# Kernel tuning notes

Hardware: AMD Instinct MI355X
Metric: run time of the kernel (lower is better)

The kernel has to match this reference:

```python
import jax, jax.numpy as jnp
import numpy as np

EMBED_DIM = 1024
NUM_HEADS = 16
HEAD_DIM = EMBED_DIM // NUM_HEADS


def setup_inputs() -> dict:
    key = jax.random.key(0)
    ks = jax.random.split(key, 7)
    B, S, D = 8, 1024, EMBED_DIM
    scale = 1.0 / np.sqrt(D)
    x = jax.random.normal(ks[0], (B, S, D), dtype=jnp.float32)
    Wq = jax.random.normal(ks[1], (D, D), dtype=jnp.float32) * scale
    Wk = jax.random.normal(ks[2], (D, D), dtype=jnp.float32) * scale
    Wv = jax.random.normal(ks[3], (D, D), dtype=jnp.float32) * scale
    bq = jax.random.normal(ks[4], (D,), dtype=jnp.float32) * 0.01
    bk = jax.random.normal(ks[5], (D,), dtype=jnp.float32) * 0.01
    bv = jax.random.normal(ks[6], (D,), dtype=jnp.float32) * 0.01
    return {"x": x, "Wq": Wq, "Wk": Wk, "Wv": Wv, "bq": bq, "bk": bk, "bv": bv}


def reference(x, Wq, Wk, Wv, bq, bk, bv):
    B, S, D = x.shape
    H, Hd = NUM_HEADS, HEAD_DIM
    # torch nn.Linear: y = x @ W.T + b
    q = (x @ Wq.T + bq).reshape(B, S, H, Hd).transpose(0, 2, 1, 3)  # [B,H,S,Hd]
    k = (x @ Wk.T + bk).reshape(B, S, H, Hd).transpose(0, 2, 1, 3)
    v = (x @ Wv.T + bv).reshape(B, S, H, Hd).transpose(0, 2, 1, 3)
    scale = Hd ** -0.5
    scores = jnp.einsum('bhqd,bhkd->bhqk', q, k) * scale  # [B,H,S,S]
    attn = jax.nn.softmax(scores, axis=-1)
    # dropout_rate = 0.0 -> identity; out_proj is never applied in the source forward
    ctx = jnp.einsum('bhqk,bhkd->bhqd', attn, v)  # [B,H,S,Hd]
    return ctx.transpose(0, 2, 1, 3).reshape(B, S, D)
```

## Files before the change

kernel.cpp:

```cpp
#include <hip/hip_runtime.h>
#include <hip/hip_bf16.h>
#include <cstdint>
#include <cstddef>


typedef __attribute__((ext_vector_type(8))) short bf16x8;
typedef __attribute__((ext_vector_type(8))) unsigned short u16x8;
typedef __attribute__((ext_vector_type(4))) float f32x4;
typedef __attribute__((ext_vector_type(16))) float f32x16;
typedef __attribute__((ext_vector_type(4))) unsigned int u32x4;
typedef __attribute__((ext_vector_type(2))) unsigned int u32x2;

typedef const __attribute__((address_space(1))) void* gptr_t;
typedef __attribute__((address_space(3))) void* lptr_t;

#define LOG2E 1.44269504088896340736f

__device__ __forceinline__ unsigned short f2bf(float f) {
  unsigned int u = __float_as_uint(f);
  u += 0x7fffu + ((u >> 16) & 1u);
  return (unsigned short)(u >> 16);
}

__device__ __forceinline__ unsigned int pack_bf16x2(float lo, float hi) {
  const __hip_bfloat162 h = __float22bfloat162_rn(float2{lo, hi});
  unsigned int u;
  __builtin_memcpy(&u, &h, 4);
  return u;
}

__device__ __forceinline__ float vmax16(const f32x16& v) {
  float a = fmaxf(fmaxf(v[0], v[1]), v[2]);
  float b = fmaxf(fmaxf(v[3], v[4]), v[5]);
  float c = fmaxf(fmaxf(v[6], v[7]), v[8]);
  float d = fmaxf(fmaxf(v[9], v[10]), v[11]);
  float e = fmaxf(fmaxf(v[12], v[13]), v[14]);
  float f = fmaxf(fmaxf(a, b), v[15]);
  float h = fmaxf(fmaxf(c, d), e);
  return fmaxf(f, h);
}

__global__ void cvt_all(const float* __restrict__ x, const float* __restrict__ wq,
                        const float* __restrict__ wk, const float* __restrict__ wv,
                        unsigned short* __restrict__ Xb, unsigned short* __restrict__ Wb) {
  const int b = blockIdx.x;
  const float* src;
  unsigned short* dst;
  int i;
  if (b < 8192) {
    src = x; dst = Xb; i = b * 256 + threadIdx.x;
  } else {
    const int s = b - 8192;
    const int sel = s >> 10;
    src = (sel == 0) ? wq : (sel == 1) ? wk : wv;
    dst = Wb + (size_t)sel * 1048576;
    i = (s & 1023) * 256 + threadIdx.x;
  }
  float4 v = reinterpret_cast<const float4*>(src)[i];
  ushort4 o;
  o.x = f2bf(v.x); o.y = f2bf(v.y); o.z = f2bf(v.z); o.w = f2bf(v.w);
  reinterpret_cast<ushort4*>(dst)[i] = o;
}

__global__ __launch_bounds__(256) void qkv_gemm(
    const unsigned short* __restrict__ Xb, const unsigned short* __restrict__ Wb,
    const float* __restrict__ bq, const float* __restrict__ bk,
    const float* __restrict__ bv,
    unsigned short* __restrict__ Qo, unsigned short* __restrict__ Ko,
    unsigned short* __restrict__ Vo) {
  __shared__ unsigned short As[128 * 32];
  __shared__ unsigned short Bs[128 * 32];

  const int tid = threadIdx.x;
  const int lane = tid & 63;
  const int w = tid >> 6;
  const int wr = w >> 1, wc = w & 1;
  const int bm = blockIdx.x & 63;
  const int bn = blockIdx.x >> 6;

  const f32x4 vzero = {0.f, 0.f, 0.f, 0.f};
  f32x4 acc[4][4];
#pragma unroll
  for (int m = 0; m < 4; ++m)
#pragma unroll
    for (int n = 0; n < 4; ++n) acc[m][n] = vzero;

  const int c0 = w * 2, c1 = w * 2 + 1;
  const int srow0 = c0 * 16 + (lane >> 2);
  const int srow1 = c1 * 16 + (lane >> 2);
  const int scol = (lane & 3) * 8;
  const unsigned short* gA0 = Xb + (size_t)(bm * 128 + srow0) * 1024 + scol;
  const unsigned short* gA1 = Xb + (size_t)(bm * 128 + srow1) * 1024 + scol;
  const unsigned short* gB0 = Wb + (size_t)(bn * 128 + srow0) * 1024 + scol;
  const unsigned short* gB1 = Wb + (size_t)(bn * 128 + srow1) * 1024 + scol;
  char* lA0 = (char*)As + c0 * 1024;
  char* lA1 = (char*)As + c1 * 1024;
  char* lB0 = (char*)Bs + c0 * 1024;
  char* lB1 = (char*)Bs + c1 * 1024;

  const int aoff = (wr * 64 + (lane & 15)) * 64 + (lane >> 4) * 16;
  const int boff = (wc * 64 + (lane & 15)) * 64 + (lane >> 4) * 16;

  for (int kt = 0; kt < 32; ++kt) {
    const int k0 = kt * 32;
    __builtin_amdgcn_global_load_lds((gptr_t)(gA0 + k0), (lptr_t)lA0, 16, 0, 0);
    __builtin_amdgcn_global_load_lds((gptr_t)(gA1 + k0), (lptr_t)lA1, 16, 0, 0);
    __builtin_amdgcn_global_load_lds((gptr_t)(gB0 + k0), (lptr_t)lB0, 16, 0, 0);
    __builtin_amdgcn_global_load_lds((gptr_t)(gB1 + k0), (lptr_t)lB1, 16, 0, 0);
    __syncthreads();

    bf16x8 a[4], b[4];
#pragma unroll
    for (int m = 0; m < 4; ++m)
      a[m] = *reinterpret_cast<const bf16x8*>((const char*)As + aoff + m * 16 * 64);
#pragma unroll
    for (int n = 0; n < 4; ++n)
      b[n] = *reinterpret_cast<const bf16x8*>((const char*)Bs + boff + n * 16 * 64);
#pragma unroll
    for (int m = 0; m < 4; ++m)
#pragma unroll
      for (int n = 0; n < 4; ++n)
        acc[m][n] = __builtin_amdgcn_mfma_f32_16x16x32_bf16(a[m], b[n], acc[m][n], 0, 0, 0);
    __syncthreads();
  }

  const int t = bn >> 3;
  const float* bias = (t == 0) ? bq : (t == 1) ? bk : bv;
  unsigned short* dst = (t == 0) ? Qo : (t == 1) ? Ko : Vo;
  const float sc = (t == 0) ? 0.125f : 1.0f;
#pragma unroll
  for (int n = 0; n < 4; ++n) {
    const int gn = bn * 128 + wc * 64 + n * 16 + (lane & 15);
    const int d = gn & 1023;
    const int h = d >> 6, hd = d & 63;
    const float bias_v = bias[d];
#pragma unroll
    for (int m = 0; m < 4; ++m) {
      const int gm0 = bm * 128 + wr * 64 + m * 16 + ((lane >> 4) << 2);
      const int bb = gm0 >> 10;
      const int s0 = gm0 & 1023;
#pragma unroll
      for (int r = 0; r < 4; ++r) {
        dst[(((size_t)bb * 16 + h) * 1024 + (size_t)(s0 + r)) * 64 + hd] =
            f2bf((acc[m][n][r] + bias_v) * sc);
      }
    }
  }
}

__global__ __launch_bounds__(256) void transpose_v(
    const unsigned short* __restrict__ Vn, unsigned short* __restrict__ Vt) {
  __shared__ __align__(16) unsigned short T[64][72];
  const int tid = threadIdx.x;
  const int head = blockIdx.x & 127;
  const int st = blockIdx.x >> 7;
  const unsigned short* src = Vn + (size_t)head * 65536 + (size_t)st * 64 * 64;
  unsigned short* dst = Vt + (size_t)head * 65536 + (size_t)st * 64;
#pragma unroll
  for (int i = 0; i < 2; ++i) {
    const int idx = tid + i * 256;
    const int r = idx >> 3, ch = idx & 7;
    u16x8 v = *reinterpret_cast<const u16x8*>(src + r * 64 + ch * 8);
#pragma unroll
    for (int j = 0; j < 8; ++j)
      T[ch * 8 + j][r ^ (ch << 3)] = (unsigned short)v[j];
  }
  __syncthreads();
#pragma unroll
  for (int i = 0; i < 2; ++i) {
    const int idx = tid + i * 256;
    const int d = idx >> 3, ch = idx & 7;
    u16x8 v = *reinterpret_cast<const u16x8*>(&T[d][(ch ^ (d >> 3)) << 3]);
    *reinterpret_cast<u16x8*>(dst + (size_t)d * 1024 + ch * 8) = v;
  }
}

__global__ __launch_bounds__(512, 4) void attn32(
    const unsigned short* __restrict__ Q, const unsigned short* __restrict__ K,
    const unsigned short* __restrict__ Vt, float* __restrict__ out) {
  __shared__ __align__(16) char smem[3][16384];

  const int tid = threadIdx.x;
  const int lane = tid & 63;
  const int ln31 = lane & 31;
  const int g = lane >> 5;
  const int w = tid >> 6;
  const int head = blockIdx.x & 127;
  const int qt = blockIdx.x >> 7;

  const unsigned short* Qh = Q + (size_t)head * 65536;
  const unsigned short* Kh = K + (size_t)head * 65536;
  const unsigned short* Vh = Vt + (size_t)head * 65536;

  const int qrow = qt * 256 + w * 32 + ln31;
  bf16x8 qf[4];
#pragma unroll
  for (int dc = 0; dc < 4; ++dc)
    qf[dc] = *reinterpret_cast<const bf16x8*>(Qh + (size_t)qrow * 64 + dc * 16 + g * 8);
  asm volatile("s_waitcnt vmcnt(0)" ::: "memory");

  const int lb = w * 1024 + lane * 16;
  const int r = lb >> 7;
  const int c = ((((lb >> 4) & 7) ^ (r & 7)) << 3);
  const unsigned short* gK = Kh + r * 64 + c;
  const unsigned short* gV = Vh + r * 1024 + c;

#pragma unroll
  for (int pt = 0; pt < 2; ++pt) {
    char* b0 = smem[pt] + w * 1024;
    __builtin_amdgcn_global_load_lds((gptr_t)(gK + pt * 4096), (lptr_t)b0, 16, 0, 0);
    __builtin_amdgcn_global_load_lds((gptr_t)(gV + pt * 64), (lptr_t)(b0 + 8192), 16, 0, 0);
  }

  float m_ = -3e38f, l_ = 0.f;
  f32x16 acc0, acc1, z16;
#pragma unroll
  for (int i = 0; i < 16; ++i) { acc0[i] = 0.f; acc1[i] = 0.f; z16[i] = 0.f; }

  const int swz = (ln31 & 7) << 4;
  const int rowb0 = ln31 * 128;
  int boff[4];
#pragma unroll
  for (int dc = 0; dc < 4; ++dc) boff[dc] = ((((dc << 1) | g) << 4) ^ swz);

  for (int kt = 0; kt < 16; ++kt) {
    if (kt < 15) {
      asm volatile("s_waitcnt vmcnt(2)" ::: "memory");
    } else {
      asm volatile("s_waitcnt vmcnt(0)" ::: "memory");
    }
    __builtin_amdgcn_s_barrier();
    __builtin_amdgcn_sched_barrier(0);

    if (kt < 14) {
      char* nb = smem[(kt + 2) % 3] + w * 1024;
      __builtin_amdgcn_global_load_lds((gptr_t)(gK + (kt + 2) * 4096), (lptr_t)nb, 16, 0, 0);
      __builtin_amdgcn_global_load_lds((gptr_t)(gV + (kt + 2) * 64), (lptr_t)(nb + 8192), 16, 0, 0);
    }

    const char* Kb_ = smem[kt % 3] + rowb0;
    const char* Vb_ = Kb_ + 8192;

    f32x16 s0, s1;
    __builtin_amdgcn_s_setprio(1);
    {
      bf16x8 kf0 = *reinterpret_cast<const bf16x8*>(Kb_ + boff[0]);
      bf16x8 kf1 = *reinterpret_cast<const bf16x8*>(Kb_ + 4096 + boff[0]);
      s0 = __builtin_amdgcn_mfma_f32_32x32x16_bf16(kf0, qf[0], z16, 0, 0, 0);
      s1 = __builtin_amdgcn_mfma_f32_32x32x16_bf16(kf1, qf[0], z16, 0, 0, 0);
    }
#pragma unroll
    for (int dc = 1; dc < 4; ++dc) {
      bf16x8 kf0 = *reinterpret_cast<const bf16x8*>(Kb_ + boff[dc]);
      bf16x8 kf1 = *reinterpret_cast<const bf16x8*>(Kb_ + 4096 + boff[dc]);
      s0 = __builtin_amdgcn_mfma_f32_32x32x16_bf16(kf0, qf[dc], s0, 0, 0, 0);
      s1 = __builtin_amdgcn_mfma_f32_32x32x16_bf16(kf1, qf[dc], s1, 0, 0, 0);
    }
    __builtin_amdgcn_s_setprio(0);

    float tm = fmaxf(vmax16(s0), vmax16(s1));
    {
      u32x2 rm = __builtin_amdgcn_permlane32_swap(
          __float_as_uint(tm), __float_as_uint(tm), false, false);
      tm = fmaxf(__uint_as_float(rm[0]), __uint_as_float(rm[1]));
    }
    if (__any(tm > m_ + 5.0f)) {
      const float mn = fmaxf(m_, tm);
      const float al = exp2f((m_ - mn) * LOG2E);
      m_ = mn;
      l_ *= al;
#pragma unroll
      for (int i = 0; i < 16; ++i) { acc0[i] *= al; acc1[i] *= al; }
    }
    const float mnl = m_ * LOG2E;
    float ts = 0.f;

    unsigned int c_[8][2];
#pragma unroll
    for (int b = 0; b < 4; ++b) {
      const float p0 = exp2f(fmaf(s0[4 * b + 0], LOG2E, -mnl));
      const float p1 = exp2f(fmaf(s0[4 * b + 1], LOG2E, -mnl));
      const float p2 = exp2f(fmaf(s0[4 * b + 2], LOG2E, -mnl));
      const float p3 = exp2f(fmaf(s0[4 * b + 3], LOG2E, -mnl));
      ts += (p0 + p1) + (p2 + p3);
      c_[b][0] = pack_bf16x2(p0, p1);
      c_[b][1] = pack_bf16x2(p2, p3);
    }
#pragma unroll
    for (int b = 4; b < 8; ++b) {
      const float p0 = exp2f(fmaf(s1[4 * (b - 4) + 0], LOG2E, -mnl));
      const float p1 = exp2f(fmaf(s1[4 * (b - 4) + 1], LOG2E, -mnl));
      const float p2 = exp2f(fmaf(s1[4 * (b - 4) + 2], LOG2E, -mnl));
      const float p3 = exp2f(fmaf(s1[4 * (b - 4) + 3], LOG2E, -mnl));
      ts += (p0 + p1) + (p2 + p3);
      c_[b][0] = pack_bf16x2(p0, p1);
      c_[b][1] = pack_bf16x2(p2, p3);
    }
    {
      u32x2 rs = __builtin_amdgcn_permlane32_swap(
          __float_as_uint(ts), __float_as_uint(ts), false, false);
      ts = __uint_as_float(rs[0]) + __uint_as_float(rs[1]);
    }
    l_ += ts;

    __builtin_amdgcn_s_setprio(1);
#pragma unroll
    for (int t = 0; t < 4; ++t) {
      u32x4 pv;
#pragma unroll
      for (int i = 0; i < 2; ++i) {
        u32x2 rr = __builtin_amdgcn_permlane32_swap(
            c_[2 * t][i], c_[2 * t + 1][i], false, false);
        pv[i] = rr[0];
        pv[i + 2] = rr[1];
      }
      const bf16x8 pfv = __builtin_bit_cast(bf16x8, pv);
      bf16x8 vf0 = *reinterpret_cast<const bf16x8*>(Vb_ + boff[t]);
      bf16x8 vf1 = *reinterpret_cast<const bf16x8*>(Vb_ + 4096 + boff[t]);
      acc0 = __builtin_amdgcn_mfma_f32_32x32x16_bf16(vf0, pfv, acc0, 0, 0, 0);
      acc1 = __builtin_amdgcn_mfma_f32_32x32x16_bf16(vf1, pfv, acc1, 0, 0, 0);
    }
    __builtin_amdgcn_s_setprio(0);
  }

  const float invl = 1.0f / l_;
  const int bb = head >> 4, hh = head & 15;
  float* orow = out + ((size_t)bb * 1024 + qrow) * 1024 + hh * 64;
#pragma unroll
  for (int rq = 0; rq < 4; ++rq) {
    const int d0 = rq * 8 + g * 4;
    float4 v0, v1;
    v0.x = acc0[rq * 4 + 0] * invl; v0.y = acc0[rq * 4 + 1] * invl;
    v0.z = acc0[rq * 4 + 2] * invl; v0.w = acc0[rq * 4 + 3] * invl;
    v1.x = acc1[rq * 4 + 0] * invl; v1.y = acc1[rq * 4 + 1] * invl;
    v1.z = acc1[rq * 4 + 2] * invl; v1.w = acc1[rq * 4 + 3] * invl;
    *reinterpret_cast<float4*>(orow + d0) = v0;
    *reinterpret_cast<float4*>(orow + 32 + d0) = v1;
  }
}

extern "C" void kernel_launch(void* const* d_in, const int* in_sizes, int n_in,
                              void* d_out, int out_size, void* d_ws, size_t ws_size,
                              hipStream_t stream) {
  const float* x  = (const float*)d_in[0];
  const float* Wq = (const float*)d_in[1];
  const float* Wk = (const float*)d_in[2];
  const float* Wv = (const float*)d_in[3];
  const float* bq = (const float*)d_in[4];
  const float* bk = (const float*)d_in[5];
  const float* bv = (const float*)d_in[6];
  float* out = (float*)d_out;

  char* ws = (char*)d_ws;
  unsigned short* Xb = (unsigned short*)(ws);
  unsigned short* Wb = (unsigned short*)(ws + (size_t)16 * 1024 * 1024);
  unsigned short* Qb = (unsigned short*)(ws + (size_t)22 * 1024 * 1024);
  unsigned short* Kb = Qb + (size_t)8 * 1024 * 1024;
  unsigned short* Vb = Kb + (size_t)8 * 1024 * 1024;
  unsigned short* Vt = Xb;

  cvt_all<<<11264, 256, 0, stream>>>(x, Wq, Wk, Wv, Xb, Wb);

  qkv_gemm<<<1536, 256, 0, stream>>>(Xb, Wb, bq, bk, bv, Qb, Kb, Vb);

  transpose_v<<<2048, 256, 0, stream>>>(Vb, Vt);

  attn32<<<512, 512, 0, stream>>>(Qb, Kb, Vt, out);
}
```

Before: 146.2 us.

## Process two 32-row query tiles per wave in attention kernel, halving block size

Each wave now handles 64 query rows, as two 32-row tiles with separate online-softmax state, instead of 32. The block shrinks from 512 to 256 threads, and each thread issues twice the K/V async LDS loads. Each K and V fragment read from LDS now feeds two MFMAs, which cuts LDS read traffic per FLOP and amortises barriers. The cost is roughly double the accumulator and score registers per thread, which lowers occupancy (launch bounds change to 256,2), so fewer waves are available to hide latency.

```diff
diff --git a/kernel.cpp b/kernel.cpp
--- a/kernel.cpp
+++ b/kernel.cpp
@@ -175,7 +175,7 @@
   }
 }
 
-__global__ __launch_bounds__(512, 4) void attn32(
+__global__ __launch_bounds__(256, 2) void attn32(
     const unsigned short* __restrict__ Q, const unsigned short* __restrict__ K,
     const unsigned short* __restrict__ Vt, float* __restrict__ out) {
   __shared__ __align__(16) char smem[3][16384];
@@ -192,30 +192,42 @@
   const unsigned short* Kh = K + (size_t)head * 65536;
   const unsigned short* Vh = Vt + (size_t)head * 65536;
 
-  const int qrow = qt * 256 + w * 32 + ln31;
-  bf16x8 qf[4];
-#pragma unroll
-  for (int dc = 0; dc < 4; ++dc)
-    qf[dc] = *reinterpret_cast<const bf16x8*>(Qh + (size_t)qrow * 64 + dc * 16 + g * 8);
+  const int qrowA = qt * 256 + w * 64 + ln31;
+  const int qrowB = qrowA + 32;
+  bf16x8 qfA[4], qfB[4];
+#pragma unroll
+  for (int dc = 0; dc < 4; ++dc) {
+    qfA[dc] = *reinterpret_cast<const bf16x8*>(Qh + (size_t)qrowA * 64 + dc * 16 + g * 8);
+    qfB[dc] = *reinterpret_cast<const bf16x8*>(Qh + (size_t)qrowB * 64 + dc * 16 + g * 8);
+  }
   asm volatile("s_waitcnt vmcnt(0)" ::: "memory");
 
-  const int lb = w * 1024 + lane * 16;
-  const int r = lb >> 7;
-  const int c = ((((lb >> 4) & 7) ^ (r & 7)) << 3);
-  const unsigned short* gK = Kh + r * 64 + c;
-  const unsigned short* gV = Vh + r * 1024 + c;
+  const int lbA = w * 1024 + lane * 16;
+  const int lbB = lbA + 4096;
+  const int rA = lbA >> 7, rB = lbB >> 7;
+  const int cA = ((((lbA >> 4) & 7) ^ (rA & 7)) << 3);
+  const int cB = ((((lbB >> 4) & 7) ^ (rB & 7)) << 3);
+  const unsigned short* gK0 = Kh + rA * 64 + cA;
+  const unsigned short* gK1 = Kh + rB * 64 + cB;
+  const unsigned short* gV0 = Vh + rA * 1024 + cA;
+  const unsigned short* gV1 = Vh + rB * 1024 + cB;
 
 #pragma unroll
   for (int pt = 0; pt < 2; ++pt) {
     char* b0 = smem[pt] + w * 1024;
-    __builtin_amdgcn_global_load_lds((gptr_t)(gK + pt * 4096), (lptr_t)b0, 16, 0, 0);
-    __builtin_amdgcn_global_load_lds((gptr_t)(gV + pt * 64), (lptr_t)(b0 + 8192), 16, 0, 0);
-  }
-
-  float m_ = -3e38f, l_ = 0.f;
-  f32x16 acc0, acc1, z16;
-#pragma unroll
-  for (int i = 0; i < 16; ++i) { acc0[i] = 0.f; acc1[i] = 0.f; z16[i] = 0.f; }
+    const int k1 = pt * 4096, k2 = pt * 64;
+    __builtin_amdgcn_global_load_lds((gptr_t)(gK0 + k1), (lptr_t)b0, 16, 0, 0);
+    __builtin_amdgcn_global_load_lds((gptr_t)(gK1 + k1), (lptr_t)(b0 + 4096), 16, 0, 0);
+    __builtin_amdgcn_global_load_lds((gptr_t)(gV0 + k2), (lptr_t)(b0 + 8192), 16, 0, 0);
+    __builtin_amdgcn_global_load_lds((gptr_t)(gV1 + k2), (lptr_t)(b0 + 12288), 16, 0, 0);
+  }
+
+  float mA = -3e38f, lA = 0.f, mB = -3e38f, lB = 0.f;
+  f32x16 accA0, accA1, accB0, accB1;
+#pragma unroll
+  for (int i = 0; i < 16; ++i) {
+    accA0[i] = 0.f; accA1[i] = 0.f; accB0[i] = 0.f; accB1[i] = 0.f;
+  }
 
   const int swz = (ln31 & 7) << 4;
   const int rowb0 = ln31 * 128;
@@ -225,7 +237,7 @@
 
   for (int kt = 0; kt < 16; ++kt) {
     if (kt < 15) {
-      asm volatile("s_waitcnt vmcnt(2)" ::: "memory");
+      asm volatile("s_waitcnt vmcnt(4)" ::: "memory");
     } else {
       asm volatile("s_waitcnt vmcnt(0)" ::: "memory");
     }
@@ -234,108 +246,137 @@
 
     if (kt < 14) {
       char* nb = smem[(kt + 2) % 3] + w * 1024;
-      __builtin_amdgcn_global_load_lds((gptr_t)(gK + (kt + 2) * 4096), (lptr_t)nb, 16, 0, 0);
-      __builtin_amdgcn_global_load_lds((gptr_t)(gV + (kt + 2) * 64), (lptr_t)(nb + 8192), 16, 0, 0);
+      const int k1 = (kt + 2) * 4096, k2 = (kt + 2) * 64;
+      __builtin_amdgcn_global_load_lds((gptr_t)(gK0 + k1), (lptr_t)nb, 16, 0, 0);
+      __builtin_amdgcn_global_load_lds((gptr_t)(gK1 + k1), (lptr_t)(nb + 4096), 16, 0, 0);
+      __builtin_amdgcn_global_load_lds((gptr_t)(gV0 + k2), (lptr_t)(nb + 8192), 16, 0, 0);
+      __builtin_amdgcn_global_load_lds((gptr_t)(gV1 + k2), (lptr_t)(nb + 12288), 16, 0, 0);
     }
 
     const char* Kb_ = smem[kt % 3] + rowb0;
     const char* Vb_ = Kb_ + 8192;
 
-    f32x16 s0, s1;
+    f32x16 sA0, sA1, sB0, sB1;
+#pragma unroll
+    for (int i = 0; i < 16; ++i) { sA0[i] = 0.f; sA1[i] = 0.f; sB0[i] = 0.f; sB1[i] = 0.f; }
     __builtin_amdgcn_s_setprio(1);
-    {
-      bf16x8 kf0 = *reinterpret_cast<const bf16x8*>(Kb_ + boff[0]);
-      bf16x8 kf1 = *reinterpret_cast<const bf16x8*>(Kb_ + 4096 + boff[0]);
-      s0 = __builtin_amdgcn_mfma_f32_32x32x16_bf16(kf0, qf[0], z16, 0, 0, 0);
-      s1 = __builtin_amdgcn_mfma_f32_32x32x16_bf16(kf1, qf[0], z16, 0, 0, 0);
-    }
-#pragma unroll
-    for (int dc = 1; dc < 4; ++dc) {
+#pragma unroll
+    for (int dc = 0; dc < 4; ++dc) {
       bf16x8 kf0 = *reinterpret_cast<const bf16x8*>(Kb_ + boff[dc]);
       bf16x8 kf1 = *reinterpret_cast<const bf16x8*>(Kb_ + 4096 + boff[dc]);
-      s0 = __builtin_amdgcn_mfma_f32_32x32x16_bf16(kf0, qf[dc], s0, 0, 0, 0);
-      s1 = __builtin_amdgcn_mfma_f32_32x32x16_bf16(kf1, qf[dc], s1, 0, 0, 0);
+      sA0 = __builtin_amdgcn_mfma_f32_32x32x16_bf16(kf0, qfA[dc], sA0, 0, 0, 0);
+      sA1 = __builtin_amdgcn_mfma_f32_32x32x16_bf16(kf1, qfA[dc], sA1, 0, 0, 0);
+      sB0 = __builtin_amdgcn_mfma_f32_32x32x16_bf16(kf0, qfB[dc], sB0, 0, 0, 0);
+      sB1 = __builtin_amdgcn_mfma_f32_32x32x16_bf16(kf1, qfB[dc], sB1, 0, 0, 0);
     }
     __builtin_amdgcn_s_setprio(0);
 
-    float tm = fmaxf(vmax16(s0), vmax16(s1));
+    float tmA = fmaxf(vmax16(sA0), vmax16(sA1));
+    float tmB = fmaxf(vmax16(sB0), vmax16(sB1));
     {
       u32x2 rm = __builtin_amdgcn_permlane32_swap(
-          __float_as_uint(tm), __float_as_uint(tm), false, false);
-      tm = fmaxf(__uint_as_float(rm[0]), __uint_as_float(rm[1]));
-    }
-    if (__any(tm > m_ + 5.0f)) {
-      const float mn = fmaxf(m_, tm);
-      const float al = exp2f((m_ - mn) * LOG2E);
-      m_ = mn;
-      l_ *= al;
-#pragma unroll
-      for (int i = 0; i < 16; ++i) { acc0[i] *= al; acc1[i] *= al; }
-    }
-    const float mnl = m_ * LOG2E;
-    float ts = 0.f;
-
-    unsigned int c_[8][2];
-#pragma unroll
-    for (int b = 0; b < 4; ++b) {
-      const float p0 = exp2f(fmaf(s0[4 * b + 0], LOG2E, -mnl));
-      const float p1 = exp2f(fmaf(s0[4 * b + 1], LOG2E, -mnl));
-      const float p2 = exp2f(fmaf(s0[4 * b + 2], LOG2E, -mnl));
-      const float p3 = exp2f(fmaf(s0[4 * b + 3], LOG2E, -mnl));
-      ts += (p0 + p1) + (p2 + p3);
-      c_[b][0] = pack_bf16x2(p0, p1);
-      c_[b][1] = pack_bf16x2(p2, p3);
-    }
-#pragma unroll
-    for (int b = 4; b < 8; ++b) {
-      const float p0 = exp2f(fmaf(s1[4 * (b - 4) + 0], LOG2E, -mnl));
-      const float p1 = exp2f(fmaf(s1[4 * (b - 4) + 1], LOG2E, -mnl));
-      const float p2 = exp2f(fmaf(s1[4 * (b - 4) + 2], LOG2E, -mnl));
-      const float p3 = exp2f(fmaf(s1[4 * (b - 4) + 3], LOG2E, -mnl));
-      ts += (p0 + p1) + (p2 + p3);
-      c_[b][0] = pack_bf16x2(p0, p1);
-      c_[b][1] = pack_bf16x2(p2, p3);
+          __float_as_uint(tmA), __float_as_uint(tmA), false, false);
+      tmA = fmaxf(__uint_as_float(rm[0]), __uint_as_float(rm[1]));
+      u32x2 rn = __builtin_amdgcn_permlane32_swap(
+          __float_as_uint(tmB), __float_as_uint(tmB), false, false);
+      tmB = fmaxf(__uint_as_float(rn[0]), __uint_as_float(rn[1]));
+    }
+    if (__any(tmA > mA + 5.0f)) {
+      const float mn = fmaxf(mA, tmA);
+      const float al = exp2f((mA - mn) * LOG2E);
+      mA = mn; lA *= al;
+#pragma unroll
+      for (int i = 0; i < 16; ++i) { accA0[i] *= al; accA1[i] *= al; }
+    }
+    if (__any(tmB > mB + 5.0f)) {
+      const float mn = fmaxf(mB, tmB);
+      const float al = exp2f((mB - mn) * LOG2E);
+      mB = mn; lB *= al;
+#pragma unroll
+      for (int i = 0; i < 16; ++i) { accB0[i] *= al; accB1[i] *= al; }
+    }
+    const float mnlA = mA * LOG2E, mnlB = mB * LOG2E;
+    float tsA = 0.f, tsB = 0.f;
+
+    unsigned int cA_[8][2], cB_[8][2];
+#pragma unroll
+    for (int b = 0; b < 8; ++b) {
+      const f32x16& sa = (b < 4) ? sA0 : sA1;
+      const f32x16& sb = (b < 4) ? sB0 : sB1;
+      const int o = (b & 3) * 4;
+      const float a0 = exp2f(fmaf(sa[o + 0], LOG2E, -mnlA));
+      const float a1 = exp2f(fmaf(sa[o + 1], LOG2E, -mnlA));
+      const float a2 = exp2f(fmaf(sa[o + 2], LOG2E, -mnlA));
+      const float a3 = exp2f(fmaf(sa[o + 3], LOG2E, -mnlA));
+      tsA += (a0 + a1) + (a2 + a3);
+      cA_[b][0] = pack_bf16x2(a0, a1);
+      cA_[b][1] = pack_bf16x2(a2, a3);
+      const float b0 = exp2f(fmaf(sb[o + 0], LOG2E, -mnlB));
+      const float b1 = exp2f(fmaf(sb[o + 1], LOG2E, -mnlB));
+      const float b2 = exp2f(fmaf(sb[o + 2], LOG2E, -mnlB));
+      const float b3 = exp2f(fmaf(sb[o + 3], LOG2E, -mnlB));
+      tsB += (b0 + b1) + (b2 + b3);
+      cB_[b][0] = pack_bf16x2(b0, b1);
+      cB_[b][1] = pack_bf16x2(b2, b3);
     }
     {
       u32x2 rs = __builtin_amdgcn_permlane32_swap(
-          __float_as_uint(ts), __float_as_uint(ts), false, false);
-      ts = __uint_as_float(rs[0]) + __uint_as_float(rs[1]);
-    }
-    l_ += ts;
+          __float_as_uint(tsA), __float_as_uint(tsA), false, false);
+      tsA = __uint_as_float(rs[0]) + __uint_as_float(rs[1]);
+      u32x2 rt = __builtin_amdgcn_permlane32_swap(
+          __float_as_uint(tsB), __float_as_uint(tsB), false, false);
+      tsB = __uint_as_float(rt[0]) + __uint_as_float(rt[1]);
+    }
+    lA += tsA;
+    lB += tsB;
 
     __builtin_amdgcn_s_setprio(1);
 #pragma unroll
     for (int t = 0; t < 4; ++t) {
-      u32x4 pv;
+      u32x4 pvA, pvB;
 #pragma unroll
       for (int i = 0; i < 2; ++i) {
-        u32x2 rr = __builtin_amdgcn_permlane32_swap(
-            c_[2 * t][i], c_[2 * t + 1][i], false, false);
-        pv[i] = rr[0];
-        pv[i + 2] = rr[1];
+        u32x2 ra = __builtin_amdgcn_permlane32_swap(
+            cA_[2 * t][i], cA_[2 * t + 1][i], false, false);
+        pvA[i] = ra[0];
+        pvA[i + 2] = ra[1];
+        u32x2 rb = __builtin_amdgcn_permlane32_swap(
+            cB_[2 * t][i], cB_[2 * t + 1][i], false, false);
+        pvB[i] = rb[0];
+        pvB[i + 2] = rb[1];
       }
-      const bf16x8 pfv = __builtin_bit_cast(bf16x8, pv);
+      const bf16x8 pfvA = __builtin_bit_cast(bf16x8, pvA);
+      const bf16x8 pfvB = __builtin_bit_cast(bf16x8, pvB);
       bf16x8 vf0 = *reinterpret_cast<const bf16x8*>(Vb_ + boff[t]);
       bf16x8 vf1 = *reinterpret_cast<const bf16x8*>(Vb_ + 4096 + boff[t]);
-      acc0 = __builtin_amdgcn_mfma_f32_32x32x16_bf16(vf0, pfv, acc0, 0, 0, 0);
-      acc1 = __builtin_amdgcn_mfma_f32_32x32x16_bf16(vf1, pfv, acc1, 0, 0, 0);
+      accA0 = __builtin_amdgcn_mfma_f32_32x32x16_bf16(vf0, pfvA, accA0, 0, 0, 0);
+      accA1 = __builtin_amdgcn_mfma_f32_32x32x16_bf16(vf1, pfvA, accA1, 0, 0, 0);
+      accB0 = __builtin_amdgcn_mfma_f32_32x32x16_bf16(vf0, pfvB, accB0, 0, 0, 0);
+      accB1 = __builtin_amdgcn_mfma_f32_32x32x16_bf16(vf1, pfvB, accB1, 0, 0, 0);
     }
     __builtin_amdgcn_s_setprio(0);
   }
 
-  const float invl = 1.0f / l_;
+  const float invlA = 1.0f / lA, invlB = 1.0f / lB;
   const int bb = head >> 4, hh = head & 15;
-  float* orow = out + ((size_t)bb * 1024 + qrow) * 1024 + hh * 64;
+  float* orowA = out + ((size_t)bb * 1024 + qrowA) * 1024 + hh * 64;
+  float* orowB = out + ((size_t)bb * 1024 + qrowB) * 1024 + hh * 64;
 #pragma unroll
   for (int rq = 0; rq < 4; ++rq) {
     const int d0 = rq * 8 + g * 4;
     float4 v0, v1;
-    v0.x = acc0[rq * 4 + 0] * invl; v0.y = acc0[rq * 4 + 1] * invl;
-    v0.z = acc0[rq * 4 + 2] * invl; v0.w = acc0[rq * 4 + 3] * invl;
-    v1.x = acc1[rq * 4 + 0] * invl; v1.y = acc1[rq * 4 + 1] * invl;
-    v1.z = acc1[rq * 4 + 2] * invl; v1.w = acc1[rq * 4 + 3] * invl;
-    *reinterpret_cast<float4*>(orow + d0) = v0;
-    *reinterpret_cast<float4*>(orow + 32 + d0) = v1;
+    v0.x = accA0[rq * 4 + 0] * invlA; v0.y = accA0[rq * 4 + 1] * invlA;
+    v0.z = accA0[rq * 4 + 2] * invlA; v0.w = accA0[rq * 4 + 3] * invlA;
+    v1.x = accA1[rq * 4 + 0] * invlA; v1.y = accA1[rq * 4 + 1] * invlA;
+    v1.z = accA1[rq * 4 + 2] * invlA; v1.w = accA1[rq * 4 + 3] * invlA;
+    *reinterpret_cast<float4*>(orowA + d0) = v0;
+    *reinterpret_cast<float4*>(orowA + 32 + d0) = v1;
+    v0.x = accB0[rq * 4 + 0] * invlB; v0.y = accB0[rq * 4 + 1] * invlB;
+    v0.z = accB0[rq * 4 + 2] * invlB; v0.w = accB0[rq * 4 + 3] * invlB;
+    v1.x = accB1[rq * 4 + 0] * invlB; v1.y = accB1[rq * 4 + 1] * invlB;
+    v1.z = accB1[rq * 4 + 2] * invlB; v1.w = accB1[rq * 4 + 3] * invlB;
+    *reinterpret_cast<float4*>(orowB + d0) = v0;
+    *reinterpret_cast<float4*>(orowB + 32 + d0) = v1;
   }
 }
 
@@ -365,5 +406,5 @@
 
   transpose_v<<<2048, 256, 0, stream>>>(Vb, Vt);
 
-  attn32<<<512, 512, 0, stream>>>(Qb, Kb, Vt, out);
-}
+  attn32<<<512, 256, 0, stream>>>(Qb, Kb, Vt, out);
+}
```

Result: slower. 151.6 us (+3.7%).
